# Performance work log

Measured on AMD Instinct MI355X. Metric: run time of the kernel, lower is better.

## Reference

```python
import jax, jax.numpy as jnp
import numpy as np

H = 1024   # hidden_size == memory_size
NH = 4     # num_attention_heads
HD = H // NH
M = 8192   # total memory items
B, S = 4, 2048
EPS = 1e-5


def _ln(x, g, b):
    mu = jnp.mean(x, -1, keepdims=True)
    var = jnp.mean((x - mu) ** 2, -1, keepdims=True)
    return (x - mu) / jnp.sqrt(var + EPS) * g + b


def setup_inputs() -> dict:
    key = jax.random.key(0)
    ks = jax.random.split(key, 16)
    s = 0.02
    return {
        "query_hidden": jax.random.normal(ks[0], (B, S, H), jnp.float32),
        "mem_keys": jax.random.normal(ks[1], (M, H), jnp.float32),
        "importance": jax.random.uniform(ks[2], (M,), jnp.float32),
        "recency": jax.random.uniform(ks[3], (M,), jnp.float32),
        "access_count": jax.random.uniform(ks[4], (M,), jnp.float32),
        "Wq": s * jax.random.normal(ks[5], (H, H), jnp.float32),
        "bq": jnp.zeros((H,), jnp.float32),
        "in_w": s * jax.random.normal(ks[6], (3 * H, H), jnp.float32),
        "in_b": jnp.zeros((3 * H,), jnp.float32),
        "out_w": s * jax.random.normal(ks[7], (H, H), jnp.float32),
        "out_b": jnp.zeros((H,), jnp.float32),
        "gate_w": s * jax.random.normal(ks[8], (H, 2 * H), jnp.float32),
        "gate_b": jnp.zeros((H,), jnp.float32),
        "int_w1": s * jax.random.normal(ks[9], (2 * H, 2 * H), jnp.float32),
        "int_b1": jnp.zeros((2 * H,), jnp.float32),
        "int_ln_g": jnp.ones((2 * H,), jnp.float32),
        "int_ln_b": jnp.zeros((2 * H,), jnp.float32),
        "int_w2": s * jax.random.normal(ks[10], (H, 2 * H), jnp.float32),
        "int_b2": jnp.zeros((H,), jnp.float32),
        "ln1_g": jnp.ones((H,), jnp.float32),
        "ln1_b": jnp.zeros((H,), jnp.float32),
        "ln2_g": jnp.ones((H,), jnp.float32),
        "ln2_b": jnp.zeros((H,), jnp.float32),
        "sel_params": jnp.ones((3,), jnp.float32) / 3.0,
        "top_k": 2048,
    }


def reference(query_hidden, mem_keys, importance, recency, access_count,
              Wq, bq, in_w, in_b, out_w, out_b, gate_w, gate_b,
              int_w1, int_b1, int_ln_g, int_ln_b, int_w2, int_b2,
              ln1_g, ln1_b, ln2_g, ln2_b, sel_params, top_k):
    b, s, _ = query_hidden.shape
    # HTPS selection: softmax-weighted mix of importance / recency / frequency
    w = jax.nn.softmax(sel_params)
    freq = access_count / jnp.max(access_count)
    sel = w[0] * importance + w[1] * recency + w[2] * freq
    _, idx = jax.lax.top_k(sel, top_k)
    mem = mem_keys[idx]                      # [K, H]
    mem_n = _ln(mem, ln1_g, ln1_b)           # layer_norm1 on memory

    q = query_hidden @ Wq.T + bq             # query_proj  [B,S,H]
    wq, wk, wv = in_w[:H], in_w[H:2 * H], in_w[2 * H:]
    bqi, bki, bvi = in_b[:H], in_b[H:2 * H], in_b[2 * H:]
    # Batched MHA: the per-position loop is equivalent to all S queries at once
    Q = (q @ wq.T + bqi).reshape(b, s, NH, HD)
    K = (mem_n @ wk.T + bki).reshape(top_k, NH, HD)   # shared across batch
    V = (mem_n @ wv.T + bvi).reshape(top_k, NH, HD)
    scores = jnp.einsum('bshd,khd->bhsk', Q, K) / jnp.sqrt(jnp.float32(HD))
    attn = jax.nn.softmax(scores, axis=-1)
    ctx = jnp.einsum('bhsk,khd->bshd', attn, V).reshape(b, s, H)
    attn_out = ctx @ out_w.T + out_b

    cat = jnp.concatenate([query_hidden, attn_out], axis=-1)   # [B,S,2H]
    gate = jax.nn.sigmoid(cat @ gate_w.T + gate_b)
    h1 = _ln(cat @ int_w1.T + int_b1, int_ln_g, int_ln_b)
    integ = jax.nn.gelu(h1, approximate=False) @ int_w2.T + int_b2
    return _ln(query_hidden + gate * integ, ln2_g, ln2_b)
```

## Files before the change

kernel.cpp:

```cpp
#include <hip/hip_runtime.h>

#define HDIM 1024
#define MMEM 8192
#define TOPK 2048
#define NROWS 8192
#define LNEPS 1e-5f

typedef unsigned short ushort_t;
typedef __bf16 bf16x8 __attribute__((ext_vector_type(8)));
typedef float f32x4 __attribute__((ext_vector_type(4)));
typedef __attribute__((address_space(1))) const void GVoid;
typedef __attribute__((address_space(3))) void LVoid;

__device__ __forceinline__ ushort_t f2bf(float f) {
    union { float f; unsigned u; } c; c.f = f;
    unsigned r = c.u + 0x7fffu + ((c.u >> 16) & 1u);
    return (ushort_t)(r >> 16);
}
__device__ __forceinline__ float bf2f(ushort_t u) {
    union { unsigned u; float f; } c; c.u = ((unsigned)u) << 16; return c.f;
}
__device__ __forceinline__ float blk_red(float v, int op, float* red) {
    #pragma unroll
    for (int o = 32; o; o >>= 1) {
        float u = __shfl_down(v, o);
        v = op ? fmaxf(v, u) : v + u;
    }
    if ((threadIdx.x & 63) == 0) red[threadIdx.x >> 6] = v;
    __syncthreads();
    float r = op ? fmaxf(fmaxf(red[0], red[1]), fmaxf(red[2], red[3]))
                 : (red[0] + red[1]) + (red[2] + red[3]);
    __syncthreads();
    return r;
}

__global__ __launch_bounds__(256) void topk_rank(const float* __restrict__ sp,
        const float* __restrict__ imp, const float* __restrict__ rec,
        const float* __restrict__ ac, int* __restrict__ idx) {
    __shared__ float s[MMEM];
    __shared__ int pc[256];
    __shared__ float red[4];
    float p0 = sp[0], p1 = sp[1], p2 = sp[2];
    float mx3 = fmaxf(p0, fmaxf(p1, p2));
    float e0 = __expf(p0 - mx3), e1 = __expf(p1 - mx3), e2 = __expf(p2 - mx3);
    float inv3 = 1.f / (e0 + e1 + e2);
    float w0 = e0 * inv3, w1 = e1 * inv3, w2 = e2 * inv3;
    float m = -1e30f;
    for (int i = threadIdx.x; i < MMEM; i += 256) m = fmaxf(m, ac[i]);
    m = blk_red(m, 1, red);
    float rinv = 1.f / m;
    for (int i = threadIdx.x; i < MMEM; i += 256)
        s[i] = w0 * imp[i] + w1 * rec[i] + w2 * (ac[i] * rinv);
    __syncthreads();
    const int li = threadIdx.x & 31;
    const int jc = threadIdx.x >> 5;
    const int i  = blockIdx.x * 32 + li;
    const float si = s[i];
    int cnt = 0;
    const float4* sv = reinterpret_cast<const float4*>(s) + jc * 256;
    #pragma unroll 4
    for (int t = 0; t < 256; ++t) {
        float4 v = sv[t];
        int j0 = jc * 1024 + t * 4;
        cnt += (v.x > si) || (v.x == si && (j0 + 0) < i);
        cnt += (v.y > si) || (v.y == si && (j0 + 1) < i);
        cnt += (v.z > si) || (v.z == si && (j0 + 2) < i);
        cnt += (v.w > si) || (v.w == si && (j0 + 3) < i);
    }
    pc[threadIdx.x] = cnt;
    __syncthreads();
    if (threadIdx.x < 32) {
        int r = 0;
        #pragma unroll
        for (int c = 0; c < 8; ++c) r += pc[c * 32 + threadIdx.x];
        if (r < TOPK) idx[r] = blockIdx.x * 32 + threadIdx.x;
    }
}

__global__ __launch_bounds__(256) void gather_ln(const float* __restrict__ mem_keys,
        const int* __restrict__ idx, const float* __restrict__ g,
        const float* __restrict__ b, ushort_t* __restrict__ out) {
    __shared__ float red[4];
    int src = idx[blockIdx.x] & (MMEM - 1);
    const float* x = mem_keys + (size_t)src * HDIM;
    float4 v = reinterpret_cast<const float4*>(x)[threadIdx.x];
    float s = v.x + v.y + v.z + v.w;
    float ss = v.x*v.x + v.y*v.y + v.z*v.z + v.w*v.w;
    s  = blk_red(s, 0, red);
    ss = blk_red(ss, 0, red);
    float mu = s * (1.f / HDIM);
    float var = ss * (1.f / HDIM) - mu * mu;
    float rstd = rsqrtf(var + LNEPS);
    int c = threadIdx.x * 4;
    ushort4 o;
    o.x = f2bf((v.x - mu) * rstd * g[c+0] + b[c+0]);
    o.y = f2bf((v.y - mu) * rstd * g[c+1] + b[c+1]);
    o.z = f2bf((v.z - mu) * rstd * g[c+2] + b[c+2]);
    o.w = f2bf((v.w - mu) * rstd * g[c+3] + b[c+3]);
    *reinterpret_cast<ushort4*>(out + (size_t)blockIdx.x * HDIM + c) = o;
}

__global__ __launch_bounds__(256) void cvt_bf16(const float* __restrict__ in,
                                                ushort_t* __restrict__ out) {
    size_t i = ((size_t)blockIdx.x * 256 + threadIdx.x) * 4;
    float4 v = *reinterpret_cast<const float4*>(in + i);
    ushort4 o = { f2bf(v.x), f2bf(v.y), f2bf(v.z), f2bf(v.w) };
    *reinterpret_cast<ushort4*>(out + i) = o;
}

__global__ __launch_bounds__(256) void cvt_all(const float* __restrict__ in_w,
        const float* __restrict__ gate_w, const float* __restrict__ int_w1,
        const float* __restrict__ int_w2,
        ushort_t* __restrict__ inw_bf, ushort_t* __restrict__ gw3,
        ushort_t* __restrict__ intw2_bf) {
    const int b = blockIdx.x;
    const float* src; ushort_t* dst; int rel;
    if      (b < 3072) { src = in_w;   dst = inw_bf;        rel = b; }
    else if (b < 5120) { src = gate_w; dst = gw3;           rel = b - 3072; }
    else if (b < 9216) { src = int_w1; dst = gw3 + 2097152; rel = b - 5120; }
    else               { src = int_w2; dst = intw2_bf;      rel = b - 9216; }
    size_t i = ((size_t)rel * 256 + threadIdx.x) * 4;
    float4 v = *reinterpret_cast<const float4*>(src + i);
    ushort4 o = { f2bf(v.x), f2bf(v.y), f2bf(v.z), f2bf(v.w) };
    *reinterpret_cast<ushort4*>(dst + i) = o;
}

__global__ __launch_bounds__(256) void cvt_t2(const float* __restrict__ a,
        const float* __restrict__ b, ushort_t* __restrict__ oa,
        ushort_t* __restrict__ ob) {
    __shared__ ushort_t t[64][65];
    const float* in = blockIdx.z ? b : a;
    ushort_t* out   = blockIdx.z ? ob : oa;
    const int bx = blockIdx.x * 64, by = blockIdx.y * 64;
    const int r = threadIdx.x >> 4, c4 = (threadIdx.x & 15) << 2;
    #pragma unroll
    for (int rr = 0; rr < 64; rr += 16) {
        float4 v = *reinterpret_cast<const float4*>(in + (size_t)(by + r + rr) * 1024 + bx + c4);
        t[r + rr][c4 + 0] = f2bf(v.x);
        t[r + rr][c4 + 1] = f2bf(v.y);
        t[r + rr][c4 + 2] = f2bf(v.z);
        t[r + rr][c4 + 3] = f2bf(v.w);
    }
    __syncthreads();
    #pragma unroll
    for (int rr = 0; rr < 64; rr += 16) {
        const int i = r + rr;
        ushort4 o = { t[c4 + 0][i], t[c4 + 1][i], t[c4 + 2][i], t[c4 + 3][i] };
        *reinterpret_cast<ushort4*>(out + (size_t)(bx + i) * 1024 + by + c4) = o;
    }
}

__global__ __launch_bounds__(256) void bias_folds(const float* __restrict__ in_w,
        const float* __restrict__ bq, const float* __restrict__ in_b,
        const float* __restrict__ gate_w, const float* __restrict__ int_w1,
        const float* __restrict__ gate_b, const float* __restrict__ int_b1,
        const float* __restrict__ out_b, float* __restrict__ beff,
        float* __restrict__ beff3) {
    __shared__ float red[4];
    const int b = blockIdx.x;
    const float* wrow; const float* vec;
    if (b < 1024) { wrow = in_w + (size_t)b * 1024; vec = bq; }
    else {
        const int j = b - 1024;
        wrow = (j < 1024 ? gate_w + (size_t)j * 2048
                         : int_w1 + (size_t)(j - 1024) * 2048) + 1024;
        vec = out_b;
    }
    const float4 wv = reinterpret_cast<const float4*>(wrow)[threadIdx.x];
    const float4 bv = reinterpret_cast<const float4*>(vec)[threadIdx.x];
    float s = wv.x*bv.x + wv.y*bv.y + wv.z*bv.z + wv.w*bv.w;
    s = blk_red(s, 0, red);
    if (threadIdx.x == 0) {
        if (b < 1024) beff[b] = s + in_b[b];
        else {
            const int j = b - 1024;
            beff3[j] = s + (j < 1024 ? gate_b[j] : int_b1[j - 1024]);
        }
    }
}

__global__ __launch_bounds__(256) void ln_gelu(ushort_t* h1,
        const float* __restrict__ g, const float* __restrict__ b) {
    __shared__ float red[4];
    ushort_t* p = h1 + (size_t)blockIdx.x * 2048 + threadIdx.x * 8;
    ushort4 a = reinterpret_cast<const ushort4*>(p)[0];
    ushort4 c = reinterpret_cast<const ushort4*>(p)[1];
    float v[8] = { bf2f(a.x), bf2f(a.y), bf2f(a.z), bf2f(a.w),
                   bf2f(c.x), bf2f(c.y), bf2f(c.z), bf2f(c.w) };
    float s = 0.f, ss = 0.f;
    #pragma unroll
    for (int j = 0; j < 8; ++j) { s += v[j]; ss += v[j]*v[j]; }
    s  = blk_red(s, 0, red);
    ss = blk_red(ss, 0, red);
    float mu = s * (1.f / 2048.f);
    float var = ss * (1.f / 2048.f) - mu * mu;
    float rstd = rsqrtf(var + LNEPS);
    int c0 = threadIdx.x * 8;
    ushort_t o[8];
    #pragma unroll
    for (int j = 0; j < 8; ++j) {
        float xn = (v[j] - mu) * rstd * g[c0 + j] + b[c0 + j];
        float ge = 0.5f * xn * (1.f + erff(xn * 0.70710678118654752f));
        o[j] = f2bf(ge);
    }
    ushort4 o1 = { o[0], o[1], o[2], o[3] };
    ushort4 o2 = { o[4], o[5], o[6], o[7] };
    reinterpret_cast<ushort4*>(p)[0] = o1;
    reinterpret_cast<ushort4*>(p)[1] = o2;
}

__global__ __launch_bounds__(256) void final_ln(const float* __restrict__ x,
        const ushort_t* __restrict__ gate, const ushort_t* __restrict__ integ,
        const float* __restrict__ g, const float* __restrict__ b,
        float* __restrict__ out) {
    __shared__ float red[4];
    size_t base = (size_t)blockIdx.x * HDIM + threadIdx.x * 4;
    float4 xv = *reinterpret_cast<const float4*>(x + base);
    ushort4 gv = *reinterpret_cast<const ushort4*>(gate + base);
    ushort4 iv = *reinterpret_cast<const ushort4*>(integ + base);
    float v[4] = { xv.x + bf2f(gv.x)*bf2f(iv.x), xv.y + bf2f(gv.y)*bf2f(iv.y),
                   xv.z + bf2f(gv.z)*bf2f(iv.z), xv.w + bf2f(gv.w)*bf2f(iv.w) };
    float s = v[0]+v[1]+v[2]+v[3];
    float ss = v[0]*v[0]+v[1]*v[1]+v[2]*v[2]+v[3]*v[3];
    s  = blk_red(s, 0, red);
    ss = blk_red(ss, 0, red);
    float mu = s * (1.f / HDIM);
    float var = ss * (1.f / HDIM) - mu * mu;
    float rstd = rsqrtf(var + LNEPS);
    int c = threadIdx.x * 4;
    float4 o;
    o.x = (v[0] - mu) * rstd * g[c+0] + b[c+0];
    o.y = (v[1] - mu) * rstd * g[c+1] + b[c+1];
    o.z = (v[2] - mu) * rstd * g[c+2] + b[c+2];
    o.w = (v[3] - mu) * rstd * g[c+3] + b[c+3];
    *reinterpret_cast<float4*>(out + base) = o;
}

template<int EPI, int BIAS, int SPLIT>
__global__ __launch_bounds__(256, 2)
void gemm_bt(const ushort_t* __restrict__ A, const ushort_t* __restrict__ B,
             const ushort_t* __restrict__ A2, const ushort_t* __restrict__ B2,
             int lda2, int ldb2,
             const float* __restrict__ bias, void* __restrict__ Cv,
             void* __restrict__ Cv2, const float* __restrict__ bias2,
             float* __restrict__ rowsum,
             int K, int lda, int ldb, int ldc,
             long long sA1, long long sA2s, long long sAz,
             long long sB1, long long sB2s, long long sBz,
             long long sC1, long long sC2s, long long sCz,
             int z2n, int zbase, float scale)
{
    __shared__ __align__(16) ushort_t As[8192];
    __shared__ __align__(16) ushort_t Bs[8192];
    const int zz = blockIdx.z;
    const int zg = zz + zbase;
    const int z1 = zg / z2n, z2 = zg - z1 * z2n;
    A += (size_t)(z1 * sA1 + z2 * sA2s + zz * sAz);
    B += (size_t)(z1 * sB1 + z2 * sB2s + zz * sBz);
    const size_t cOff = (size_t)(z1 * sC1 + z2 * sC2s + zz * sCz);

    const int nwg = gridDim.x * gridDim.y;
    const int wg  = blockIdx.y * gridDim.x + blockIdx.x;
    const int q8  = nwg >> 3, r8 = nwg & 7;
    const int xcd = wg & 7, lo = wg >> 3;
    const int wgid = (xcd < r8 ? xcd * (q8 + 1) : r8 * (q8 + 1) + (xcd - r8) * q8) + lo;
    const int m0 = (wgid / gridDim.x) * 128, n0 = (wgid % gridDim.x) * 128;

    const int tid = threadIdx.x;
    const int w = tid >> 6, l = tid & 63;
    const int wm = w >> 1, wn = w & 1;

    f32x4 acc[4][4] = {};
    const int srow = l >> 3;
    const int scol = ((l & 7) ^ srow) << 3;

    for (int k0 = 0; k0 < K; k0 += 64) {
        const ushort_t* Ab = A; const ushort_t* Bb = B;
        int la = lda, lb = ldb, kk0 = k0;
        if (SPLIT && k0 >= 1024) { Ab = A2; Bb = B2; la = lda2; lb = ldb2; kk0 = k0 - 1024; }
        #pragma unroll
        for (int i = 0; i < 4; ++i) {
            const int c = i * 4 + w;
            const int row = c * 8 + srow;
            const ushort_t* ga = Ab + (size_t)(m0 + row) * la + (kk0 + scol);
            const ushort_t* gb = Bb + (size_t)(n0 + row) * lb + (kk0 + scol);
            __builtin_amdgcn_global_load_lds((GVoid*)ga, (LVoid*)(As + c * 512), 16, 0, 0);
            __builtin_amdgcn_global_load_lds((GVoid*)gb, (LVoid*)(Bs + c * 512), 16, 0, 0);
        }
        __syncthreads();
        #pragma unroll
        for (int kk = 0; kk < 2; ++kk) {
            bf16x8 af[4], bfv[4];
            #pragma unroll
            for (int m = 0; m < 4; ++m) {
                const int row = wm * 64 + m * 16 + (l & 15);
                const int cb = ((kk * 64) + ((l >> 4) * 16)) ^ ((row & 7) << 4);
                af[m] = *reinterpret_cast<const bf16x8*>(
                    reinterpret_cast<const char*>(As) + row * 128 + cb);
            }
            #pragma unroll
            for (int n = 0; n < 4; ++n) {
                const int row = wn * 64 + n * 16 + (l & 15);
                const int cb = ((kk * 64) + ((l >> 4) * 16)) ^ ((row & 7) << 4);
                bfv[n] = *reinterpret_cast<const bf16x8*>(
                    reinterpret_cast<const char*>(Bs) + row * 128 + cb);
            }
            #pragma unroll
            for (int m = 0; m < 4; ++m)
                #pragma unroll
                for (int n = 0; n < 4; ++n)
                    acc[m][n] = __builtin_amdgcn_mfma_f32_16x16x32_bf16(
                        af[m], bfv[n], acc[m][n], 0, 0, 0);
        }
        __syncthreads();
    }

    if (EPI == 4) {
        float* rs = reinterpret_cast<float*>(As);
        for (int t = tid; t < 128; t += 256) rs[t] = 0.f;
        __syncthreads();
        #pragma unroll
        for (int m = 0; m < 4; ++m) {
            const int rl = wm * 64 + m * 16 + ((l >> 4) << 2);
            float psum[4] = {0.f, 0.f, 0.f, 0.f};
            #pragma unroll
            for (int n = 0; n < 4; ++n) {
                const int gcol = n0 + wn * 64 + n * 16 + (l & 15);
                #pragma unroll
                for (int j = 0; j < 4; ++j) {
                    float e = __expf(acc[m][n][j] * scale);
                    ((ushort_t*)Cv)[cOff + (size_t)(m0 + rl + j) * ldc + gcol] = f2bf(e);
                    psum[j] += e;
                }
            }
            #pragma unroll
            for (int j = 0; j < 4; ++j) atomicAdd(&rs[rl + j], psum[j]);
        }
        __syncthreads();
        for (int t = tid; t < 128; t += 256)
            atomicAdd(rowsum + (size_t)zg * 2048 + m0 + t, rs[t]);
        return;
    }

    #pragma unroll
    for (int m = 0; m < 4; ++m) {
        const int grow = m0 + wm * 64 + m * 16 + ((l >> 4) << 2);
        float rsc[4];
        if (BIAS == 3) {
            #pragma unroll
            for (int j = 0; j < 4; ++j)
                rsc[j] = 1.f / rowsum[(size_t)zg * 2048 + grow + j];
        }
        #pragma unroll
        for (int n = 0; n < 4; ++n) {
            const int gcol = n0 + wn * 64 + n * 16 + (l & 15);
            float bc = (BIAS == 1) ? bias[gcol] : 0.f;
            #pragma unroll
            for (int j = 0; j < 4; ++j) {
                if (EPI == 3) {
                    float v = acc[m][n][j];
                    if (gcol < 1024) {
                        v += bias[gcol];
                        v = 1.f / (1.f + __expf(-v));
                        ((ushort_t*)Cv)[(size_t)(grow + j) * ldc + gcol] = f2bf(v);
                    } else {
                        v += bias2[gcol - 1024];
                        ((ushort_t*)Cv2)[(size_t)(grow + j) * 2048 + (gcol - 1024)] = f2bf(v);
                    }
                } else {
                    float v = acc[m][n][j] * scale;
                    if (BIAS == 1) v += bc;
                    if (BIAS == 2) v += bias[grow + j];
                    if (BIAS == 3) v *= rsc[j];
                    const size_t off = cOff + (size_t)(grow + j) * ldc + gcol;
                    if (EPI == 1) ((ushort_t*)Cv)[off] = f2bf(v);
                    else          ((float*)Cv)[off]    = v;
                }
            }
        }
    }
}

extern "C" void kernel_launch(void* const* d_in, const int* in_sizes, int n_in,
                              void* d_out, int out_size, void* d_ws, size_t ws_size,
                              hipStream_t stream) {
    const float* x          = (const float*)d_in[0];
    const float* mem_keys   = (const float*)d_in[1];
    const float* importance = (const float*)d_in[2];
    const float* recency    = (const float*)d_in[3];
    const float* access_cnt = (const float*)d_in[4];
    const float* Wq         = (const float*)d_in[5];
    const float* bq         = (const float*)d_in[6];
    const float* in_w       = (const float*)d_in[7];
    const float* in_b       = (const float*)d_in[8];
    const float* out_w      = (const float*)d_in[9];
    const float* out_b      = (const float*)d_in[10];
    const float* gate_w     = (const float*)d_in[11];
    const float* gate_b     = (const float*)d_in[12];
    const float* int_w1     = (const float*)d_in[13];
    const float* int_b1     = (const float*)d_in[14];
    const float* int_ln_g   = (const float*)d_in[15];
    const float* int_ln_b   = (const float*)d_in[16];
    const float* int_w2     = (const float*)d_in[17];
    const float* int_b2     = (const float*)d_in[18];
    const float* ln1_g      = (const float*)d_in[19];
    const float* ln1_b      = (const float*)d_in[20];
    const float* ln2_g      = (const float*)d_in[21];
    const float* ln2_b      = (const float*)d_in[22];
    const float* sel_params = (const float*)d_in[23];

    char* ws = (char*)d_ws;
    size_t off = 0;
    auto alloc = [&](size_t bytes) -> char* {
        char* p = ws + off;
        off = (off + bytes + 255) & ~(size_t)255;
        return p;
    };

    int*      idx      = (int*)alloc(TOPK * 4);
    float*    beff     = (float*)alloc(1024 * 4);
    float*    beff3    = (float*)alloc(3072 * 4);
    float*    rowsum   = (float*)alloc((size_t)16 * 2048 * 4);
    ushort_t* wqT_bf   = (ushort_t*)alloc((size_t)1048576 * 2);
    ushort_t* outwT_bf = (ushort_t*)alloc((size_t)1048576 * 2);
    ushort_t* weff_bf  = (ushort_t*)alloc((size_t)1048576 * 2);
    ushort_t* inw_bf   = (ushort_t*)alloc((size_t)3145728 * 2);
    ushort_t* gw3      = (ushort_t*)alloc((size_t)6291456 * 2);
    ushort_t* wfold3   = (ushort_t*)alloc((size_t)3145728 * 2);
    ushort_t* intw2_bf = (ushort_t*)alloc((size_t)2097152 * 2);
    ushort_t* mem_n    = (ushort_t*)alloc((size_t)TOPK * HDIM * 2);
    ushort_t* Kbuf     = (ushort_t*)alloc((size_t)TOPK * HDIM * 2);
    ushort_t* Vt       = (ushort_t*)alloc((size_t)HDIM * TOPK * 2);
    ushort_t* xbf      = (ushort_t*)alloc((size_t)NROWS * HDIM * 2);
    ushort_t* qQ       = (ushort_t*)alloc((size_t)NROWS * 2048 * 2);
    ushort_t* Qbuf     = qQ + (size_t)NROWS * HDIM;
    ushort_t* h1       = qQ;
    ushort_t* ctx      = (ushort_t*)alloc((size_t)NROWS * HDIM * 2);
    ushort_t* integ    = ctx;

    int NC = 16;
    while (NC > 1 && off + (size_t)NC * 8388608 > ws_size) NC >>= 1;
    ushort_t* scores = (ushort_t*)alloc((size_t)NC * 8388608);
    ushort_t* gatev  = scores;

    cvt_t2<<<dim3(16,16,2), 256, 0, stream>>>(Wq, out_w, wqT_bf, outwT_bf);
    cvt_all<<<11264, 256, 0, stream>>>(in_w, gate_w, int_w1, int_w2,
                                       inw_bf, gw3, intw2_bf);
    cvt_bf16<<<8192, 256, 0, stream>>>(x, xbf);
    bias_folds<<<4096, 256, 0, stream>>>(in_w, bq, in_b, gate_w, int_w1,
                                         gate_b, int_b1, out_b, beff, beff3);

    gemm_bt<1,0,0><<<dim3(8,8,1), 256, 0, stream>>>(inw_bf, wqT_bf,
        nullptr, nullptr, 0, 0, nullptr, weff_bf, nullptr, nullptr, nullptr,
        1024, 1024, 1024, 1024, 0,0,0, 0,0,0, 0,0,0, 1, 0, 1.f);
    gemm_bt<1,0,0><<<dim3(8,24,1), 256, 0, stream>>>(gw3 + 1024, outwT_bf,
        nullptr, nullptr, 0, 0, nullptr, wfold3, nullptr, nullptr, nullptr,
        1024, 2048, 1024, 1024, 0,0,0, 0,0,0, 0,0,0, 1, 0, 1.f);

    topk_rank<<<MMEM/32, 256, 0, stream>>>(sel_params, importance, recency,
                                           access_cnt, idx);
    gather_ln<<<TOPK, 256, 0, stream>>>(mem_keys, idx, ln1_g, ln1_b, mem_n);

    gemm_bt<1,1,0><<<dim3(8,64,1), 256, 0, stream>>>(xbf, weff_bf,
        nullptr, nullptr, 0, 0, beff, Qbuf, nullptr, nullptr, nullptr,
        1024, 1024, 1024, 1024, 0,0,0, 0,0,0, 0,0,0, 1, 0, 1.f);
    gemm_bt<1,1,0><<<dim3(8,16,1), 256, 0, stream>>>(mem_n, inw_bf + 1048576,
        nullptr, nullptr, 0, 0, in_b + 1024, Kbuf, nullptr, nullptr, nullptr,
        1024, 1024, 1024, 1024, 0,0,0, 0,0,0, 0,0,0, 1, 0, 1.f);
    gemm_bt<1,2,0><<<dim3(16,8,1), 256, 0, stream>>>(inw_bf + 2097152, mem_n,
        nullptr, nullptr, 0, 0, in_b + 2048, Vt, nullptr, nullptr, nullptr,
        1024, 1024, 1024, 2048, 0,0,0, 0,0,0, 0,0,0, 1, 0, 1.f);

    hipMemsetAsync(rowsum, 0, (size_t)16 * 2048 * 4, stream);

    for (int c0 = 0; c0 < 16; c0 += NC) {
        gemm_bt<4,0,0><<<dim3(16,16,NC), 256, 0, stream>>>(Qbuf, Kbuf,
            nullptr, nullptr, 0, 0, nullptr, scores, nullptr, nullptr, rowsum,
            256, 1024, 1024, 2048,
            2097152, 256, 0,  0, 256, 0,  0, 0, 4194304, 4, c0, 0.0625f);
        gemm_bt<1,3,0><<<dim3(2,16,NC), 256, 0, stream>>>(scores, Vt,
            nullptr, nullptr, 0, 0, nullptr, ctx, nullptr, nullptr, rowsum,
            2048, 2048, 2048, 1024,
            0, 0, 4194304,  0, 524288, 0,  2097152, 256, 0, 4, c0, 1.f);
    }

    gemm_bt<3,0,1><<<dim3(24,64,1), 256, 0, stream>>>(xbf, gw3,
        ctx, wfold3, 1024, 1024, beff3, gatev, h1, beff3 + 1024, nullptr,
        2048, 1024, 2048, 1024, 0,0,0, 0,0,0, 0,0,0, 1, 0, 1.f);

    ln_gelu<<<NROWS, 256, 0, stream>>>(h1, int_ln_g, int_ln_b);
    gemm_bt<1,1,0><<<dim3(8,64,1), 256, 0, stream>>>(h1, intw2_bf,
        nullptr, nullptr, 0, 0, int_b2, integ, nullptr, nullptr, nullptr,
        2048, 2048, 2048, 1024, 0,0,0, 0,0,0, 0,0,0, 1, 0, 1.f);
    final_ln<<<NROWS, 256, 0, stream>>>(x, gatev, integ, ln2_g, ln2_b, (float*)d_out);
}
```

Baseline: 610.4 us.

## Fuse QK^T, exp, row-sum and PV into one flash-style attention kernel

The two-pass attention is replaced with a single kernel, `fattn`. The old path wrote bf16 exp-scores to global memory, accumulated row sums with global atomics, then ran a separate PV GEMM. The new kernel keeps each 64x128 probability tile in LDS, accumulates row sums in shared memory and normalises the output in its epilogue. This removes the large scores round trip through HBM, the rowsum memset and the chunked launch loop. In exchange it uses small 64-row tiles, reloads the Q tile for every key chunk and has no software pipelining, which may leave the matrix units less fully used than the old GEMM path.

```diff
diff --git a/kernel.cpp b/kernel.cpp
--- a/kernel.cpp
+++ b/kernel.cpp
@@ -236,6 +236,152 @@
     *reinterpret_cast<float4*>(out + base) = o;
 }
 
+__global__ __launch_bounds__(256, 2)
+void fattn(const ushort_t* __restrict__ Q, const ushort_t* __restrict__ Kb,
+           const ushort_t* __restrict__ Vt, ushort_t* __restrict__ ctx)
+{
+    __shared__ __align__(16) ushort_t Pb[8192];
+    __shared__ __align__(16) ushort_t Stg[16384];
+    __shared__ float rsum[64];
+
+    const int z1 = blockIdx.y >> 2, z2 = blockIdx.y & 3;
+    const int m0 = blockIdx.x * 64;
+    const ushort_t* Qp = Q  + (size_t)z1 * 2097152 + z2 * 256;
+    const ushort_t* Kp = Kb + z2 * 256;
+    const ushort_t* Vp = Vt + (size_t)z2 * 524288;
+
+    const int tid = threadIdx.x;
+    const int w = tid >> 6, l = tid & 63;
+    const int srow = l >> 3;
+    const int scol = ((l & 7) ^ srow) << 3;
+    const int l15 = l & 15, lh = l >> 4;
+
+    if (tid < 64) rsum[tid] = 0.f;
+
+    f32x4 oacc[4][4] = {};
+
+    for (int ch = 0; ch < 16; ++ch) {
+        f32x4 sacc[4][2] = {};
+        for (int k0 = 0; k0 < 256; k0 += 64) {
+            #pragma unroll
+            for (int i = 0; i < 2; ++i) {
+                const int c = i * 4 + w;
+                const ushort_t* g = Qp + (size_t)(m0 + c * 8 + srow) * 1024 + k0 + scol;
+                __builtin_amdgcn_global_load_lds((GVoid*)g, (LVoid*)(Stg + c * 512), 16, 0, 0);
+            }
+            #pragma unroll
+            for (int i = 0; i < 4; ++i) {
+                const int c = i * 4 + w;
+                const ushort_t* g = Kp + (size_t)(ch * 128 + c * 8 + srow) * 1024 + k0 + scol;
+                __builtin_amdgcn_global_load_lds((GVoid*)g, (LVoid*)(Stg + 4096 + c * 512), 16, 0, 0);
+            }
+            __syncthreads();
+            #pragma unroll
+            for (int kk = 0; kk < 2; ++kk) {
+                bf16x8 af[4], bv[2];
+                #pragma unroll
+                for (int m = 0; m < 4; ++m) {
+                    const int row = m * 16 + l15;
+                    const int cb = ((kk * 64) + lh * 16) ^ ((row & 7) << 4);
+                    af[m] = *reinterpret_cast<const bf16x8*>(
+                        reinterpret_cast<const char*>(Stg) + row * 128 + cb);
+                }
+                #pragma unroll
+                for (int n = 0; n < 2; ++n) {
+                    const int row = w * 32 + n * 16 + l15;
+                    const int cb = ((kk * 64) + lh * 16) ^ ((row & 7) << 4);
+                    bv[n] = *reinterpret_cast<const bf16x8*>(
+                        reinterpret_cast<const char*>(Stg) + 8192 + row * 128 + cb);
+                }
+                #pragma unroll
+                for (int m = 0; m < 4; ++m)
+                    #pragma unroll
+                    for (int n = 0; n < 2; ++n)
+                        sacc[m][n] = __builtin_amdgcn_mfma_f32_16x16x32_bf16(
+                            af[m], bv[n], sacc[m][n], 0, 0, 0);
+            }
+            __syncthreads();
+        }
+        #pragma unroll
+        for (int m = 0; m < 4; ++m) {
+            float ps[4] = {0.f, 0.f, 0.f, 0.f};
+            #pragma unroll
+            for (int n = 0; n < 2; ++n) {
+                const int pcol = w * 32 + n * 16 + l15;
+                #pragma unroll
+                for (int j = 0; j < 4; ++j) {
+                    const int prow = m * 16 + lh * 4 + j;
+                    float e = __expf(sacc[m][n][j] * 0.0625f);
+                    ps[j] += e;
+                    const int cb = (pcol * 2) ^ ((prow & 7) << 4);
+                    *reinterpret_cast<ushort_t*>(
+                        reinterpret_cast<char*>(Pb) + prow * 256 + cb) = f2bf(e);
+                }
+            }
+            #pragma unroll
+            for (int j = 0; j < 4; ++j) {
+                float s = ps[j];
+                s += __shfl_xor(s, 1); s += __shfl_xor(s, 2);
+                s += __shfl_xor(s, 4); s += __shfl_xor(s, 8);
+                if (l15 == 0) atomicAdd(&rsum[m * 16 + lh * 4 + j], s);
+            }
+        }
+        #pragma unroll
+        for (int ks = 0; ks < 128; ks += 64) {
+            #pragma unroll
+            for (int i = 0; i < 8; ++i) {
+                const int c = i * 4 + w;
+                const ushort_t* g = Vp + (size_t)(c * 8 + srow) * 2048 + ch * 128 + ks + scol;
+                __builtin_amdgcn_global_load_lds((GVoid*)g, (LVoid*)(Stg + c * 512), 16, 0, 0);
+            }
+            __syncthreads();
+            #pragma unroll
+            for (int kk = 0; kk < 2; ++kk) {
+                bf16x8 pa[4], vb[4];
+                #pragma unroll
+                for (int m = 0; m < 4; ++m) {
+                    const int row = m * 16 + l15;
+                    const int cb = (ks * 2 + kk * 64 + lh * 16) ^ ((row & 7) << 4);
+                    pa[m] = *reinterpret_cast<const bf16x8*>(
+                        reinterpret_cast<const char*>(Pb) + row * 256 + cb);
+                }
+                #pragma unroll
+                for (int n = 0; n < 4; ++n) {
+                    const int row = w * 64 + n * 16 + l15;
+                    const int cb = ((kk * 64) + lh * 16) ^ ((row & 7) << 4);
+                    vb[n] = *reinterpret_cast<const bf16x8*>(
+                        reinterpret_cast<const char*>(Stg) + row * 128 + cb);
+                }
+                #pragma unroll
+                for (int m = 0; m < 4; ++m)
+                    #pragma unroll
+                    for (int n = 0; n < 4; ++n)
+                        oacc[m][n] = __builtin_amdgcn_mfma_f32_16x16x32_bf16(
+                            pa[m], vb[n], oacc[m][n], 0, 0, 0);
+            }
+            __syncthreads();
+        }
+    }
+
+    #pragma unroll
+    for (int m = 0; m < 4; ++m) {
+        float riv[4];
+        #pragma unroll
+        for (int j = 0; j < 4; ++j)
+            riv[j] = 1.f / rsum[m * 16 + lh * 4 + j];
+        #pragma unroll
+        for (int n = 0; n < 4; ++n) {
+            const int dcol = w * 64 + n * 16 + l15;
+            #pragma unroll
+            for (int j = 0; j < 4; ++j) {
+                const int row = m * 16 + lh * 4 + j;
+                const size_t off = (size_t)(z1 * 2048 + m0 + row) * 1024 + z2 * 256 + dcol;
+                ctx[off] = f2bf(oacc[m][n][j] * riv[j]);
+            }
+        }
+    }
+}
+
 template<int EPI, int BIAS, int SPLIT>
 __global__ __launch_bounds__(256, 2)
 void gemm_bt(const ushort_t* __restrict__ A, const ushort_t* __restrict__ B,
@@ -243,7 +389,6 @@
              int lda2, int ldb2,
              const float* __restrict__ bias, void* __restrict__ Cv,
              void* __restrict__ Cv2, const float* __restrict__ bias2,
-             float* __restrict__ rowsum,
              int K, int lda, int ldb, int ldc,
              long long sA1, long long sA2s, long long sAz,
              long long sB1, long long sB2s, long long sBz,
@@ -315,42 +460,9 @@
         __syncthreads();
     }
 
-    if (EPI == 4) {
-        float* rs = reinterpret_cast<float*>(As);
-        for (int t = tid; t < 128; t += 256) rs[t] = 0.f;
-        __syncthreads();
-        #pragma unroll
-        for (int m = 0; m < 4; ++m) {
-            const int rl = wm * 64 + m * 16 + ((l >> 4) << 2);
-            float psum[4] = {0.f, 0.f, 0.f, 0.f};
-            #pragma unroll
-            for (int n = 0; n < 4; ++n) {
-                const int gcol = n0 + wn * 64 + n * 16 + (l & 15);
-                #pragma unroll
-                for (int j = 0; j < 4; ++j) {
-                    float e = __expf(acc[m][n][j] * scale);
-                    ((ushort_t*)Cv)[cOff + (size_t)(m0 + rl + j) * ldc + gcol] = f2bf(e);
-                    psum[j] += e;
-                }
-            }
-            #pragma unroll
-            for (int j = 0; j < 4; ++j) atomicAdd(&rs[rl + j], psum[j]);
-        }
-        __syncthreads();
-        for (int t = tid; t < 128; t += 256)
-            atomicAdd(rowsum + (size_t)zg * 2048 + m0 + t, rs[t]);
-        return;
-    }
-
     #pragma unroll
     for (int m = 0; m < 4; ++m) {
         const int grow = m0 + wm * 64 + m * 16 + ((l >> 4) << 2);
-        float rsc[4];
-        if (BIAS == 3) {
-            #pragma unroll
-            for (int j = 0; j < 4; ++j)
-                rsc[j] = 1.f / rowsum[(size_t)zg * 2048 + grow + j];
-        }
         #pragma unroll
         for (int n = 0; n < 4; ++n) {
             const int gcol = n0 + wn * 64 + n * 16 + (l & 15);
@@ -371,7 +483,7 @@
                     float v = acc[m][n][j] * scale;
                     if (BIAS == 1) v += bc;
                     if (BIAS == 2) v += bias[grow + j];
-                    if (BIAS == 3) v *= rsc[j];
+                    if (EPI == 2) v = 1.f / (1.f + __expf(-v));
                     const size_t off = cOff + (size_t)(grow + j) * ldc + gcol;
                     if (EPI == 1) ((ushort_t*)Cv)[off] = f2bf(v);
                     else          ((float*)Cv)[off]    = v;
@@ -420,7 +532,6 @@
     int*      idx      = (int*)alloc(TOPK * 4);
     float*    beff     = (float*)alloc(1024 * 4);
     float*    beff3    = (float*)alloc(3072 * 4);
-    float*    rowsum   = (float*)alloc((size_t)16 * 2048 * 4);
     ushort_t* wqT_bf   = (ushort_t*)alloc((size_t)1048576 * 2);
     ushort_t* outwT_bf = (ushort_t*)alloc((size_t)1048576 * 2);
     ushort_t* weff_bf  = (ushort_t*)alloc((size_t)1048576 * 2);
@@ -432,16 +543,11 @@
     ushort_t* Kbuf     = (ushort_t*)alloc((size_t)TOPK * HDIM * 2);
     ushort_t* Vt       = (ushort_t*)alloc((size_t)HDIM * TOPK * 2);
     ushort_t* xbf      = (ushort_t*)alloc((size_t)NROWS * HDIM * 2);
-    ushort_t* qQ       = (ushort_t*)alloc((size_t)NROWS * 2048 * 2);
-    ushort_t* Qbuf     = qQ + (size_t)NROWS * HDIM;
-    ushort_t* h1       = qQ;
+    ushort_t* Qbuf     = (ushort_t*)alloc((size_t)NROWS * HDIM * 2);
+    ushort_t* h1       = (ushort_t*)alloc((size_t)NROWS * 2048 * 2);
     ushort_t* ctx      = (ushort_t*)alloc((size_t)NROWS * HDIM * 2);
     ushort_t* integ    = ctx;
-
-    int NC = 16;
-    while (NC > 1 && off + (size_t)NC * 8388608 > ws_size) NC >>= 1;
-    ushort_t* scores = (ushort_t*)alloc((size_t)NC * 8388608);
-    ushort_t* gatev  = scores;
+    ushort_t* gatev    = (ushort_t*)alloc((size_t)NROWS * HDIM * 2);
 
     cvt_t2<<<dim3(16,16,2), 256, 0, stream>>>(Wq, out_w, wqT_bf, outwT_bf);
     cvt_all<<<11264, 256, 0, stream>>>(in_w, gate_w, int_w1, int_w2,
@@ -451,10 +557,10 @@
                                          gate_b, int_b1, out_b, beff, beff3);
 
     gemm_bt<1,0,0><<<dim3(8,8,1), 256, 0, stream>>>(inw_bf, wqT_bf,
-        nullptr, nullptr, 0, 0, nullptr, weff_bf, nullptr, nullptr, nullptr,
+        nullptr, nullptr, 0, 0, nullptr, weff_bf, nullptr, nullptr,
         1024, 1024, 1024, 1024, 0,0,0, 0,0,0, 0,0,0, 1, 0, 1.f);
     gemm_bt<1,0,0><<<dim3(8,24,1), 256, 0, stream>>>(gw3 + 1024, outwT_bf,
-        nullptr, nullptr, 0, 0, nullptr, wfold3, nullptr, nullptr, nullptr,
+        nullptr, nullptr, 0, 0, nullptr, wfold3, nullptr, nullptr,
         1024, 2048, 1024, 1024, 0,0,0, 0,0,0, 0,0,0, 1, 0, 1.f);
 
     topk_rank<<<MMEM/32, 256, 0, stream>>>(sel_params, importance, recency,
@@ -462,35 +568,24 @@
     gather_ln<<<TOPK, 256, 0, stream>>>(mem_keys, idx, ln1_g, ln1_b, mem_n);
 
     gemm_bt<1,1,0><<<dim3(8,64,1), 256, 0, stream>>>(xbf, weff_bf,
-        nullptr, nullptr, 0, 0, beff, Qbuf, nullptr, nullptr, nullptr,
+        nullptr, nullptr, 0, 0, beff, Qbuf, nullptr, nullptr,
         1024, 1024, 1024, 1024, 0,0,0, 0,0,0, 0,0,0, 1, 0, 1.f);
     gemm_bt<1,1,0><<<dim3(8,16,1), 256, 0, stream>>>(mem_n, inw_bf + 1048576,
-        nullptr, nullptr, 0, 0, in_b + 1024, Kbuf, nullptr, nullptr, nullptr,
+        nullptr, nullptr, 0, 0, in_b + 1024, Kbuf, nullptr, nullptr,
         1024, 1024, 1024, 1024, 0,0,0, 0,0,0, 0,0,0, 1, 0, 1.f);
     gemm_bt<1,2,0><<<dim3(16,8,1), 256, 0, stream>>>(inw_bf + 2097152, mem_n,
-        nullptr, nullptr, 0, 0, in_b + 2048, Vt, nullptr, nullptr, nullptr,
+        nullptr, nullptr, 0, 0, in_b + 2048, Vt, nullptr, nullptr,
         1024, 1024, 1024, 2048, 0,0,0, 0,0,0, 0,0,0, 1, 0, 1.f);
 
-    hipMemsetAsync(rowsum, 0, (size_t)16 * 2048 * 4, stream);
-
-    for (int c0 = 0; c0 < 16; c0 += NC) {
-        gemm_bt<4,0,0><<<dim3(16,16,NC), 256, 0, stream>>>(Qbuf, Kbuf,
-            nullptr, nullptr, 0, 0, nullptr, scores, nullptr, nullptr, rowsum,
-            256, 1024, 1024, 2048,
-            2097152, 256, 0,  0, 256, 0,  0, 0, 4194304, 4, c0, 0.0625f);
-        gemm_bt<1,3,0><<<dim3(2,16,NC), 256, 0, stream>>>(scores, Vt,
-            nullptr, nullptr, 0, 0, nullptr, ctx, nullptr, nullptr, rowsum,
-            2048, 2048, 2048, 1024,
-            0, 0, 4194304,  0, 524288, 0,  2097152, 256, 0, 4, c0, 1.f);
-    }
+    fattn<<<dim3(32,16), 256, 0, stream>>>(Qbuf, Kbuf, Vt, ctx);
 
     gemm_bt<3,0,1><<<dim3(24,64,1), 256, 0, stream>>>(xbf, gw3,
-        ctx, wfold3, 1024, 1024, beff3, gatev, h1, beff3 + 1024, nullptr,
+        ctx, wfold3, 1024, 1024, beff3, gatev, h1, beff3 + 1024,
         2048, 1024, 2048, 1024, 0,0,0, 0,0,0, 0,0,0, 1, 0, 1.f);
 
     ln_gelu<<<NROWS, 256, 0, stream>>>(h1, int_ln_g, int_ln_b);
     gemm_bt<1,1,0><<<dim3(8,64,1), 256, 0, stream>>>(h1, intw2_bf,
-        nullptr, nullptr, 0, 0, int_b2, integ, nullptr, nullptr, nullptr,
+        nullptr, nullptr, 0, 0, int_b2, integ, nullptr, nullptr,
         2048, 2048, 2048, 1024, 0,0,0, 0,0,0, 0,0,0, 1, 0, 1.f);
     final_ln<<<NROWS, 256, 0, stream>>>(x, gatev, integ, ln2_g, ln2_b, (float*)d_out);
 }
```

Result: faster. 541.4 us (-11.3%).
